# Kernel tuning notes

Measured on AMD Instinct MI355X. Metric: run time of the kernel, lower is better.

## Reference

```python
import jax, jax.numpy as jnp
import numpy as np

N_HEADS = 16

def setup_inputs() -> dict:
    key = jax.random.key(0)
    k1, k2, k3 = jax.random.split(key, 3)
    B, T, C = 4, 2048, 1024
    x = jax.random.normal(k1, (B, T, C), dtype=jnp.float32)
    W_kqv = jax.random.normal(k2, (C, 3 * C), dtype=jnp.float32) * (C ** -0.5)
    W_proj = jax.random.normal(k3, (C, C), dtype=jnp.float32) * (C ** -0.5)
    return {"x": x, "W_kqv": W_kqv, "W_proj": W_proj}


def reference(x, W_kqv, W_proj):
    # x: (B,T,C). Dropout layers are identity in eval mode (p treated as 0).
    B, T, C = x.shape
    H = N_HEADS
    D = C // H
    dk = D ** -0.5
    kqv = x @ W_kqv                     # (B,T,3C)
    kqv = kqv.reshape(B, T, 3, H, D).transpose(2, 0, 3, 1, 4)  # (3,B,H,T,D)
    k, q, v = kqv[0], kqv[1], kqv[2]    # note: k first, matching source
    scores = jnp.einsum('bhqd,bhkd->bhqk', q, k) * dk  # (B,H,T,T)
    attn = jax.nn.softmax(scores, axis=-1)
    out = jnp.einsum('bhqk,bhkd->bhqd', attn, v)       # (B,H,T,D)
    out = out.transpose(0, 2, 1, 3).reshape(B, T, C)   # (B,T,C)
    return out @ W_proj
```

## Files before the change

kernel.cpp:

```cpp
#include <hip/hip_runtime.h>
#include <hip/hip_bf16.h>

typedef unsigned short ushort_t;
typedef __attribute__((ext_vector_type(8))) short short8;
typedef __attribute__((ext_vector_type(4))) float f32x4;

__device__ __forceinline__ ushort_t f2bf(float f) {
    union { float f; unsigned int u; } v; v.f = f;
    unsigned int r = v.u + 0x7fffu + ((v.u >> 16) & 1u);
    return (ushort_t)(r >> 16);
}

__device__ __forceinline__ unsigned int cvtpk(float lo, float hi) {
    unsigned int r;
    asm("v_cvt_pk_bf16_f32 %0, %1, %2" : "=v"(r) : "v"(lo), "v"(hi));
    return r;
}

__device__ __forceinline__ void async16(const ushort_t* g, ushort_t* l) {
    __builtin_amdgcn_global_load_lds((const __attribute__((address_space(1))) void*)g,
                                     (__attribute__((address_space(3))) void*)l,
                                     16, 0, 0);
}

__global__ void cvt_bf16(const float* __restrict__ src, ushort_t* __restrict__ dst) {
    int i = (blockIdx.x * 256 + threadIdx.x) * 8;
    float4 f0 = *(const float4*)(src + i);
    float4 f1 = *(const float4*)(src + i + 4);
    union { uint4 v; ushort_t e[8]; } d;
    d.e[0]=f2bf(f0.x); d.e[1]=f2bf(f0.y); d.e[2]=f2bf(f0.z); d.e[3]=f2bf(f0.w);
    d.e[4]=f2bf(f1.x); d.e[5]=f2bf(f1.y); d.e[6]=f2bf(f1.z); d.e[7]=f2bf(f1.w);
    *(uint4*)(dst + i) = d.v;
}

__global__ void transpose_w(const float* __restrict__ src, ushort_t* __restrict__ dst,
                            int R, int C, int lo, int hi, float scale) {
    __shared__ ushort_t tile[32][33];
    const int bx = blockIdx.x * 32, by = blockIdx.y * 32;
    const int tx = threadIdx.x, ty = threadIdx.y;
    const float s = (bx + tx >= lo && bx + tx < hi) ? scale : 1.0f;
    #pragma unroll
    for (int i = 0; i < 32; i += 8)
        tile[ty + i][tx] = f2bf(src[(size_t)(by + ty + i) * C + bx + tx] * s);
    __syncthreads();
    #pragma unroll
    for (int i = 0; i < 32; i += 8)
        dst[(size_t)(bx + ty + i) * R + by + tx] = tile[tx][ty + i];
}

__global__ void transpose_v(const ushort_t* __restrict__ kqv, ushort_t* __restrict__ vT) {
    __shared__ ushort_t tile[32][33];
    const int bh = blockIdx.z;
    const int b = bh >> 4, h = bh & 15;
    const int t0 = blockIdx.x * 32, d0 = blockIdx.y * 32;
    const int tx = threadIdx.x, ty = threadIdx.y;
    #pragma unroll
    for (int i = 0; i < 32; i += 8)
        tile[ty + i][tx] = kqv[(size_t)(b * 2048 + t0 + ty + i) * 3072 + 2048 + h * 64 + d0 + tx];
    __syncthreads();
    #pragma unroll
    for (int i = 0; i < 32; i += 8)
        vT[((size_t)bh * 64 + d0 + ty + i) * 2048 + t0 + tx] = tile[tx][ty + i];
}

template <bool CF32>
__global__ __launch_bounds__(256, 2)
void gemm_bt(const ushort_t* __restrict__ A, const ushort_t* __restrict__ Bt,
             void* __restrict__ Cv, int M, int N, int K) {
    constexpr int BK = 32;
    __shared__ ushort_t As[128 * BK];
    __shared__ ushort_t Bs[128 * BK];

    const int tid  = threadIdx.x;
    const int wave = tid >> 6;
    const int lane = tid & 63;
    const int quad = lane >> 4;
    const int l16  = lane & 15;
    const int m0 = blockIdx.x * 128;
    const int n0 = blockIdx.y * 128;
    const int wm = (wave >> 1) * 64;
    const int wn = (wave & 1) * 64;
    const int rA = (lane >> 2);
    const int cA = (lane & 3) * 8;

    f32x4 acc[4][4] = {};

    for (int k0 = 0; k0 < K; k0 += BK) {
        __syncthreads();
        #pragma unroll
        for (int u = 0; u < 2; ++u) {
            int c = wave * 2 + u;
            int row = c * 16 + rA;
            async16(A  + (size_t)(m0 + row) * K + k0 + cA, As + c * 512);
            async16(Bt + (size_t)(n0 + row) * K + k0 + cA, Bs + c * 512);
        }
        __syncthreads();

        short8 af[4], bf[4];
        #pragma unroll
        for (int mt = 0; mt < 4; ++mt)
            af[mt] = *(const short8*)(As + (wm + mt * 16 + l16) * BK + quad * 8);
        #pragma unroll
        for (int nt = 0; nt < 4; ++nt)
            bf[nt] = *(const short8*)(Bs + (wn + nt * 16 + l16) * BK + quad * 8);

        #pragma unroll
        for (int mt = 0; mt < 4; ++mt)
            #pragma unroll
            for (int nt = 0; nt < 4; ++nt)
                acc[mt][nt] = __builtin_amdgcn_mfma_f32_16x16x32_bf16(
                    af[mt], bf[nt], acc[mt][nt], 0, 0, 0);
    }

    #pragma unroll
    for (int mt = 0; mt < 4; ++mt) {
        #pragma unroll
        for (int r = 0; r < 4; ++r) {
            int row = m0 + wm + mt * 16 + quad * 4 + r;
            if constexpr (CF32) {
                float* op = (float*)Cv + (size_t)row * N + n0 + wn + l16;
                #pragma unroll
                for (int nt = 0; nt < 4; ++nt) op[nt * 16] = acc[mt][nt][r];
            } else {
                ushort_t* op = (ushort_t*)Cv + (size_t)row * N + n0 + wn + l16;
                #pragma unroll
                for (int nt = 0; nt < 4; ++nt) op[nt * 16] = f2bf(acc[mt][nt][r]);
            }
        }
    }
}

__global__ __launch_bounds__(256, 3)
void attn_kernel(const ushort_t* __restrict__ kqv, const ushort_t* __restrict__ vT,
                 ushort_t* __restrict__ aout) {
    constexpr int T = 2048;
    constexpr int NT = T / 64;

    __shared__ __align__(16) ushort_t smem[24576];
    ushort_t* const Ps = smem + 16384;

    const int tid  = threadIdx.x;
    const int wave = tid >> 6;
    const int lane = tid & 63;
    const int quad = lane >> 4;
    const int l16  = lane & 15;

    const int lin = blockIdx.x;
    const int qt  = (lin >> 3) & 15;
    const int bh  = ((lin >> 7) << 3) | (lin & 7);
    const int b   = bh >> 4, h = bh & 15;
    const int q0  = qt * 128;
    const size_t rowBase = (size_t)b * T;

    short8 qf[2][2];
    #pragma unroll
    for (int mt = 0; mt < 2; ++mt) {
        const ushort_t* qp = kqv + (rowBase + q0 + wave * 32 + mt * 16 + l16) * 3072 + 1024 + h * 64;
        qf[mt][0] = *(const short8*)(qp + quad * 8);
        qf[mt][1] = *(const short8*)(qp + 32 + quad * 8);
    }

    const ushort_t* kbase = kqv + rowBase * 3072 + h * 64;
    const ushort_t* vbase = vT + (size_t)bh * 64 * 2048;
    ushort_t* const pw = Ps + wave * 2048;

    const int swz = l16 & 7;
    const int qh  = quad >> 1;
    int wrow[2], gxo[4];
    #pragma unroll
    for (int mt = 0; mt < 2; ++mt) wrow[mt] = (mt * 16 + l16) * 64 + (quad & 1) * 4;
    #pragma unroll
    for (int nt = 0; nt < 4; ++nt) gxo[nt] = ((nt * 2 + qh) ^ swz) * 8;

    auto stage = [&](ushort_t* dk, ushort_t* dv, int kk) {
        #pragma unroll
        for (int u = 0; u < 2; ++u) {
            int g = u * 256 + tid;
            int row = g >> 3, pos = g & 7;
            int c = pos ^ (row & 7);
            async16(kbase + (size_t)(kk + row) * 3072 + c * 8, dk + g * 8);
            async16(vbase + (size_t)row * 2048 + kk + c * 8, dv + g * 8);
        }
    };

    f32x4 O[2][4] = {};
    float lrow[2] = {};

    stage(smem, smem + 4096, 0);

    #pragma unroll 2
    for (int t = 0; t < NT; ++t) {
        ushort_t* const Ks = smem + ((t & 1) << 13);
        ushort_t* const Vs = Ks + 4096;
        ushort_t* const Kn = smem + (((t & 1) ^ 1) << 13);

        __builtin_amdgcn_s_barrier();
        if (t + 1 < NT) {
            stage(Kn, Kn + 4096, (t + 1) * 64);
            asm volatile("s_waitcnt vmcnt(4)" ::: "memory");
        } else {
            asm volatile("s_waitcnt vmcnt(0)" ::: "memory");
        }
        __builtin_amdgcn_s_barrier();
        __builtin_amdgcn_sched_barrier(0);

        f32x4 S[2][4];
        #pragma unroll
        for (int nt = 0; nt < 4; ++nt) {
            int key = nt * 16 + l16;
            const ushort_t* kr = Ks + key * 64;
            short8 kf0 = *(const short8*)(kr + ((quad     ^ (l16 & 7)) * 8));
            short8 kf1 = *(const short8*)(kr + (((quad+4) ^ (l16 & 7)) * 8));
            #pragma unroll
            for (int mt = 0; mt < 2; ++mt) {
                f32x4 s = {0.f, 0.f, 0.f, 0.f};
                s = __builtin_amdgcn_mfma_f32_16x16x32_bf16(kf0, qf[mt][0], s, 0, 0, 0);
                s = __builtin_amdgcn_mfma_f32_16x16x32_bf16(kf1, qf[mt][1], s, 0, 0, 0);
                S[mt][nt] = s;
            }
        }

        #pragma unroll
        for (int mt = 0; mt < 2; ++mt) {
            #pragma unroll
            for (int nt = 0; nt < 4; ++nt) {
                float p0 = __builtin_amdgcn_exp2f(S[mt][nt][0]);
                float p1 = __builtin_amdgcn_exp2f(S[mt][nt][1]);
                float p2 = __builtin_amdgcn_exp2f(S[mt][nt][2]);
                float p3 = __builtin_amdgcn_exp2f(S[mt][nt][3]);
                lrow[mt] += (p0 + p1) + (p2 + p3);
                uint2 w;
                w.x = cvtpk(p0, p1);
                w.y = cvtpk(p2, p3);
                *(uint2*)(pw + wrow[mt] + gxo[nt]) = w;
            }
        }
        asm volatile("s_waitcnt lgkmcnt(0)" ::: "memory");

        short8 pf[2][2];
        #pragma unroll
        for (int mt = 0; mt < 2; ++mt)
            #pragma unroll
            for (int f = 0; f < 2; ++f)
                pf[mt][f] = *(const short8*)(pw + (mt * 16 + l16) * 64 + (((f * 4 + quad) ^ swz) * 8));

        #pragma unroll
        for (int dt = 0; dt < 4; ++dt) {
            int d = dt * 16 + l16;
            const ushort_t* vr = Vs + d * 64;
            short8 vf0 = *(const short8*)(vr + ((quad     ^ (l16 & 7)) * 8));
            short8 vf1 = *(const short8*)(vr + (((quad+4) ^ (l16 & 7)) * 8));
            #pragma unroll
            for (int mt = 0; mt < 2; ++mt) {
                O[mt][dt] = __builtin_amdgcn_mfma_f32_16x16x32_bf16(pf[mt][0], vf0, O[mt][dt], 0, 0, 0);
                O[mt][dt] = __builtin_amdgcn_mfma_f32_16x16x32_bf16(pf[mt][1], vf1, O[mt][dt], 0, 0, 0);
            }
        }
    }

    #pragma unroll
    for (int mt = 0; mt < 2; ++mt) {
        float s = lrow[mt];
        s += __shfl_xor(s, 16, 64);
        s += __shfl_xor(s, 32, 64);
        float inv[4];
        #pragma unroll
        for (int r = 0; r < 4; ++r)
            inv[r] = 1.f / __shfl(s, quad * 4 + r, 64);
        #pragma unroll
        for (int dt = 0; dt < 4; ++dt)
            #pragma unroll
            for (int r = 0; r < 4; ++r) {
                int row = q0 + wave * 32 + mt * 16 + quad * 4 + r;
                aout[(rowBase + row) * 1024 + h * 64 + dt * 16 + l16] = f2bf(O[mt][dt][r] * inv[r]);
            }
    }
}

extern "C" void kernel_launch(void* const* d_in, const int* in_sizes, int n_in,
                              void* d_out, int out_size, void* d_ws, size_t ws_size,
                              hipStream_t stream) {
    const float* x     = (const float*)d_in[0];
    const float* Wkqv  = (const float*)d_in[1];
    const float* Wproj = (const float*)d_in[2];
    float* out = (float*)d_out;

    constexpr int M = 8192, K = 1024;
    constexpr float SC = 0.18033688011112042f;
    char* ws = (char*)d_ws;
    ushort_t* kqv    = (ushort_t*)(ws);
    ushort_t* vT     = (ushort_t*)(ws + 50331648);
    ushort_t* xb     = (ushort_t*)(ws + 67108864);
    ushort_t* aout   = xb;
    ushort_t* WkqvT  = (ushort_t*)(ws + 83886080);
    ushort_t* WprojT = (ushort_t*)(ws + 90177536);

    cvt_bf16<<<4096, 256, 0, stream>>>(x, xb);
    transpose_w<<<dim3(96, 32), dim3(32, 8), 0, stream>>>(Wkqv, WkqvT, 1024, 3072, 1024, 2048, SC);
    transpose_w<<<dim3(32, 32), dim3(32, 8), 0, stream>>>(Wproj, WprojT, 1024, 1024, 0, 0, 1.0f);

    gemm_bt<false><<<dim3(M / 128, 3072 / 128), 256, 0, stream>>>(xb, WkqvT, kqv, M, 3072, K);
    transpose_v<<<dim3(64, 2, 64), dim3(32, 8), 0, stream>>>(kqv, vT);
    attn_kernel<<<1024, 256, 0, stream>>>(kqv, vT, aout);
    gemm_bt<true><<<dim3(M / 128, 1024 / 128), 256, 0, stream>>>(aout, WprojT, out, M, 1024, K);
}
```

Baseline: 267.3 us.

## Fuse V transpose into QKV GEMM epilogue, remap workgroups, add MFMA priority

The QKV GEMM now writes the V columns directly in transposed (b,h,d,t) layout through an LDS staging tile, which removes the separate transpose_v kernel and its extra read and write of V. Workgroup indices are remapped so that consecutive blocks are spread across groups of eight, likely to improve cache locality across XCDs. The attention kernel raises wave priority around its MFMA sections with s_setprio. Together these add epilogue complexity and extra barriers to the GEMM blocks that handle V.

Measured after the change: 279.3 us. 1.04x slower.

```diff
diff --git a/kernel.cpp b/kernel.cpp
--- a/kernel.cpp
+++ b/kernel.cpp
@@ -48,25 +48,10 @@
         dst[(size_t)(bx + ty + i) * R + by + tx] = tile[tx][ty + i];
 }
 
-__global__ void transpose_v(const ushort_t* __restrict__ kqv, ushort_t* __restrict__ vT) {
-    __shared__ ushort_t tile[32][33];
-    const int bh = blockIdx.z;
-    const int b = bh >> 4, h = bh & 15;
-    const int t0 = blockIdx.x * 32, d0 = blockIdx.y * 32;
-    const int tx = threadIdx.x, ty = threadIdx.y;
-    #pragma unroll
-    for (int i = 0; i < 32; i += 8)
-        tile[ty + i][tx] = kqv[(size_t)(b * 2048 + t0 + ty + i) * 3072 + 2048 + h * 64 + d0 + tx];
-    __syncthreads();
-    #pragma unroll
-    for (int i = 0; i < 32; i += 8)
-        vT[((size_t)bh * 64 + d0 + ty + i) * 2048 + t0 + tx] = tile[tx][ty + i];
-}
-
-template <bool CF32>
+template <bool CF32, bool VOUT>
 __global__ __launch_bounds__(256, 2)
 void gemm_bt(const ushort_t* __restrict__ A, const ushort_t* __restrict__ Bt,
-             void* __restrict__ Cv, int M, int N, int K) {
+             void* __restrict__ Cv, ushort_t* __restrict__ vT, int M, int N, int K) {
     constexpr int BK = 32;
     __shared__ ushort_t As[128 * BK];
     __shared__ ushort_t Bs[128 * BK];
@@ -76,8 +61,14 @@
     const int lane = tid & 63;
     const int quad = lane >> 4;
     const int l16  = lane & 15;
-    const int m0 = blockIdx.x * 128;
-    const int n0 = blockIdx.y * 128;
+
+    const int gdx = gridDim.x;
+    const int nwg = gdx * gridDim.y;
+    int lin = blockIdx.y * gdx + blockIdx.x;
+    int wg  = (nwg & 7) ? lin : ((lin & 7) * (nwg >> 3) + (lin >> 3));
+    const int m0 = (wg % gdx) * 128;
+    const int n0 = (wg / gdx) * 128;
+
     const int wm = (wave >> 1) * 64;
     const int wn = (wave & 1) * 64;
     const int rA = (lane >> 2);
@@ -110,6 +101,43 @@
             for (int nt = 0; nt < 4; ++nt)
                 acc[mt][nt] = __builtin_amdgcn_mfma_f32_16x16x32_bf16(
                     af[mt], bf[nt], acc[mt][nt], 0, 0, 0);
+    }
+
+    if constexpr (VOUT) {
+        if (n0 >= 2048) {
+            const int b  = m0 >> 11;
+            const int tb = m0 & 2047;
+            const int h0 = (n0 - 2048) >> 6;
+            ushort_t* tileT = As;
+            __syncthreads();
+            #pragma unroll
+            for (int hh = 0; hh < 2; ++hh) {
+                if ((wave & 1) == hh) {
+                    #pragma unroll
+                    for (int nt = 0; nt < 4; ++nt) {
+                        int d = nt * 16 + l16;
+                        #pragma unroll
+                        for (int mt = 0; mt < 4; ++mt) {
+                            int t = wm + mt * 16 + quad * 4;
+                            uint2 w;
+                            w.x = cvtpk(acc[mt][nt][0], acc[mt][nt][1]);
+                            w.y = cvtpk(acc[mt][nt][2], acc[mt][nt][3]);
+                            *(uint2*)(tileT + d * 128 + t) = w;
+                        }
+                    }
+                }
+                __syncthreads();
+                #pragma unroll
+                for (int i = 0; i < 4; ++i) {
+                    int c = i * 256 + tid;
+                    int d = c >> 4, cp = (c & 15) * 8;
+                    *(uint4*)(vT + ((size_t)((b * 16 + h0 + hh) * 64 + d)) * 2048 + tb + cp) =
+                        *(const uint4*)(tileT + d * 128 + cp);
+                }
+                __syncthreads();
+            }
+            return;
+        }
     }
 
     #pragma unroll
@@ -205,6 +233,7 @@
         __builtin_amdgcn_sched_barrier(0);
 
         f32x4 S[2][4];
+        __builtin_amdgcn_s_setprio(1);
         #pragma unroll
         for (int nt = 0; nt < 4; ++nt) {
             int key = nt * 16 + l16;
@@ -219,6 +248,7 @@
                 S[mt][nt] = s;
             }
         }
+        __builtin_amdgcn_s_setprio(0);
 
         #pragma unroll
         for (int mt = 0; mt < 2; ++mt) {
@@ -244,6 +274,7 @@
             for (int f = 0; f < 2; ++f)
                 pf[mt][f] = *(const short8*)(pw + (mt * 16 + l16) * 64 + (((f * 4 + quad) ^ swz) * 8));
 
+        __builtin_amdgcn_s_setprio(1);
         #pragma unroll
         for (int dt = 0; dt < 4; ++dt) {
             int d = dt * 16 + l16;
@@ -256,6 +287,7 @@
                 O[mt][dt] = __builtin_amdgcn_mfma_f32_16x16x32_bf16(pf[mt][1], vf1, O[mt][dt], 0, 0, 0);
             }
         }
+        __builtin_amdgcn_s_setprio(0);
     }
 
     #pragma unroll
@@ -299,8 +331,7 @@
     transpose_w<<<dim3(96, 32), dim3(32, 8), 0, stream>>>(Wkqv, WkqvT, 1024, 3072, 1024, 2048, SC);
     transpose_w<<<dim3(32, 32), dim3(32, 8), 0, stream>>>(Wproj, WprojT, 1024, 1024, 0, 0, 1.0f);
 
-    gemm_bt<false><<<dim3(M / 128, 3072 / 128), 256, 0, stream>>>(xb, WkqvT, kqv, M, 3072, K);
-    transpose_v<<<dim3(64, 2, 64), dim3(32, 8), 0, stream>>>(kqv, vT);
+    gemm_bt<false, true><<<dim3(M / 128, 3072 / 128), 256, 0, stream>>>(xb, WkqvT, kqv, vT, M, 3072, K);
     attn_kernel<<<1024, 256, 0, stream>>>(kqv, vT, aout);
-    gemm_bt<true><<<dim3(M / 128, 1024 / 128), 256, 0, stream>>>(aout, WprojT, out, M, 1024, K);
-}
+    gemm_bt<true, false><<<dim3(M / 128, 1024 / 128), 256, 0, stream>>>(aout, WprojT, out, nullptr, M, 1024, K);
+}
```
